# Performance work log

Hardware: AMD Instinct MI355X
Metric: run time of the kernel (lower is better)

Reference implementation:

```python
import jax, jax.numpy as jnp
import numpy as np
import math

N, E, LAT, MUL, HD = 20000, 160000, 128, 16, 32
H = LAT // HD          # 4 heads
D = 9                  # 0e+1o+2e spherical harmonics dim
SLICES = ((0, 1), (1, 4), (4, 9))
TPD = MUL * len(SLICES)


def _mlp(x, W1, b1, W2, b2):
    return jnp.dot(jax.nn.silu(jnp.dot(x, W1) + b1), W2) + b2


def _eq_linear(x, W):
    # block-diagonal per-l channel mixing: x [E, mul, D], W [n_l, mul, mul]
    return jnp.concatenate([jnp.einsum('ji,eim->ejm', W[l], x[:, :, s:t])
                            for l, (s, t) in enumerate(SLICES)], axis=-1)


def _residual(x, x_new, uc):
    co = jax.lax.rsqrt(uc * uc + 1.0)
    return co * x + (uc * co) * x_new


def _vec_rej(feat, dirs):
    d = dirs[:, None, :]
    return feat - (feat * d).sum(-1, keepdims=True) * d


def _so3_ln(x, eps=1e-8):
    # equivariant RMS layernorm per irrep block
    out = []
    for s, t in SLICES:
        blk = x[:, :, s:t]
        rms = jnp.sqrt((blk * blk).sum(-1).mean(-1) + eps)  # [N]
        out.append(blk / rms[:, None, None])
    return jnp.concatenate(out, axis=-1)


def _ln(x, g, b, eps=1e-5):
    mu = x.mean(-1, keepdims=True)
    var = ((x - mu) ** 2).mean(-1, keepdims=True)
    return (x - mu) * jax.lax.rsqrt(var + eps) * g + b


def _forward(h, X, t_ij, spharms, update_coeff, Wtq, Wtk, Wrs_W, Wrs_b, Wq_W, Wq_b, Wk_W, Wk_b, Wre_W, ln_g, ln_b, Wvu,
             gs_W1, gs_b1, gs_W2, gs_b2, gv_W1, gv_b1, gv_W2, gv_b2, gw_W1, gw_b1, gw_W2, gw_b2,
             gt_W1, gt_b1, gt_W2, gt_b2, gsp_W1, gsp_b1, gsp_W2, gsp_b2, md_W1, md_b1, md_W2, md_b2,
             mt_W1, mt_b1, mt_W2, mt_b2, gm_W1, gm_b1, gm_W2, gm_b2,
             edge_center, edge_neighbor, num_nodes):
    uc = update_coeff
    Xn = X[edge_neighbor]                                     # [E, mul, D]
    Xq = _vec_rej(_eq_linear(X[edge_center], Wtq), spharms)
    Xk = _vec_rej(_eq_linear(Xn, Wtk), -spharms)
    # CG scalar contraction (l x l -> 0e, uuu): normalized per-l dot product
    w = jnp.concatenate([(Xq[:, :, s:t] * Xk[:, :, s:t]).sum(-1) / math.sqrt(t - s)
                         for s, t in SLICES], axis=-1)        # [E, 3*mul]
    dt = _mlp(w, gw_W1, gw_b1, gw_W2, gw_b2) * _mlp(t_ij, gt_W1, gt_b1, gt_W2, gt_b2)
    t_ij = _residual(t_ij, dt, uc)
    h_i = h[edge_center]
    h_j = h[edge_neighbor]
    spatial = (t_ij @ Wrs_W + Wrs_b) * _mlp(h_j, gs_W1, gs_b1, gs_W2, gs_b2)
    En = t_ij.shape[0]
    q = (h_i @ Wq_W + Wq_b).reshape(En, H, HD)
    k = (h_j @ Wk_W + Wk_b).reshape(En, H, HD)
    v = _mlp(h_j, gv_W1, gv_b1, gv_W2, gv_b2)
    ta = jax.nn.silu(t_ij @ Wre_W).reshape(En, H, HD)
    alpha = (q * k * ta).sum(-1) / math.sqrt(HD)              # [E, H]
    amax = jax.ops.segment_max(alpha, edge_center, num_segments=num_nodes)
    ex = jnp.exp(alpha - amax[edge_center])
    den = jax.ops.segment_sum(ex, edge_center, num_segments=num_nodes)
    attn = ex / den[edge_center]                              # scatter_softmax
    sea = (attn[:, :, None] * v.reshape(En, H, HD)).reshape(En, LAT)
    combined = sea + spatial
    gates = _mlp(combined, gsp_W1, gsp_b1, gsp_W2, gsp_b2)
    o_s, o_d, o_t = gates[:, :LAT], gates[:, LAT:2 * LAT], gates[:, 2 * LAT:]
    dh = _ln(jax.ops.segment_sum(o_s, edge_center, num_segments=num_nodes), ln_g, ln_b)
    h = _residual(h, dh, uc)
    gd = _mlp(o_d, md_W1, md_b1, md_W2, md_b2)
    gtt = _mlp(o_t, mt_W1, mt_b1, mt_W2, mt_b2)
    dXij = gd[:, :, None] * spharms[:, None, :] + gtt[:, :, None] * Xn
    dX = _so3_ln(jax.ops.segment_sum(dXij, edge_center, num_segments=num_nodes))
    X = _residual(X, dX, uc)
    # EQFF
    Xp = jnp.einsum('nmi,mj->nji', X, Wvu)
    nrm = jnp.sqrt((Xp * Xp).sum(-1) + 1e-12)
    g = _mlp(jnp.concatenate([h, nrm], axis=-1), gm_W1, gm_b1, gm_W2, gm_b2)
    h = h + g[:, :LAT]
    X = X + g[:, LAT:, None] * Xp
    return h, X, t_ij


def setup_inputs() -> dict:
    key = jax.random.key(0)
    ks = jax.random.split(key, 24)

    def mk_mlp(k, din, dout):
        k1, k2 = jax.random.split(k)
        return (jax.random.normal(k1, (din, LAT)) / math.sqrt(din), jnp.zeros((LAT,)),
                jax.random.normal(k2, (LAT, dout)) / math.sqrt(LAT), jnp.zeros((dout,)))

    inp = {
        'h': jax.random.normal(ks[0], (N, LAT)),
        'X': jax.random.normal(ks[1], (N, MUL, D)),
        't_ij': jax.random.normal(ks[2], (E, LAT)),
        'spharms': jax.random.normal(ks[3], (E, D)),
        'update_coeff': jnp.ones((1,), dtype=jnp.float32),
        'Wtq': jax.random.normal(ks[4], (len(SLICES), MUL, MUL)) / math.sqrt(MUL),
        'Wtk': jax.random.normal(ks[5], (len(SLICES), MUL, MUL)) / math.sqrt(MUL),
        'Wrs_W': jax.random.normal(ks[6], (LAT, LAT)) / math.sqrt(LAT),
        'Wrs_b': jnp.zeros((LAT,)),
        'Wq_W': jax.random.normal(ks[7], (LAT, LAT)) / math.sqrt(LAT),
        'Wq_b': jnp.zeros((LAT,)),
        'Wk_W': jax.random.normal(ks[8], (LAT, LAT)) / math.sqrt(LAT),
        'Wk_b': jnp.zeros((LAT,)),
        'Wre_W': jax.random.normal(ks[9], (LAT, LAT)) / math.sqrt(LAT),
        'ln_g': jnp.ones((LAT,)),
        'ln_b': jnp.zeros((LAT,)),
        'Wvu': jax.random.normal(ks[10], (MUL, MUL)) / math.sqrt(MUL),
    }
    for name, din, dout, k in [('gs', LAT, LAT, ks[11]), ('gv', LAT, LAT, ks[12]), ('gw', TPD, LAT, ks[13]),
                               ('gt', LAT, LAT, ks[14]), ('gsp', LAT, 3 * LAT, ks[15]), ('md', LAT, MUL, ks[16]),
                               ('mt', LAT, MUL, ks[17]), ('gm', LAT + MUL, LAT + MUL, ks[18])]:
        W1, b1, W2, b2 = mk_mlp(k, din, dout)
        inp[name + '_W1'], inp[name + '_b1'], inp[name + '_W2'], inp[name + '_b2'] = W1, b1, W2, b2
    inp['edge_center'] = jax.random.randint(ks[19], (E,), 0, N)
    inp['edge_neighbor'] = jax.random.randint(ks[20], (E,), 0, N)
    inp['num_nodes'] = N
    return inp


def reference(h, X, t_ij, spharms, update_coeff, Wtq, Wtk, Wrs_W, Wrs_b, Wq_W, Wq_b, Wk_W, Wk_b, Wre_W, ln_g, ln_b, Wvu,
              gs_W1, gs_b1, gs_W2, gs_b2, gv_W1, gv_b1, gv_W2, gv_b2, gw_W1, gw_b1, gw_W2, gw_b2,
              gt_W1, gt_b1, gt_W2, gt_b2, gsp_W1, gsp_b1, gsp_W2, gsp_b2, md_W1, md_b1, md_W2, md_b2,
              mt_W1, mt_b1, mt_W2, mt_b2, gm_W1, gm_b1, gm_W2, gm_b2,
              edge_center, edge_neighbor, num_nodes):
    return _forward(h, X, t_ij, spharms, update_coeff, Wtq, Wtk, Wrs_W, Wrs_b, Wq_W, Wq_b, Wk_W, Wk_b, Wre_W, ln_g, ln_b, Wvu,
                    gs_W1, gs_b1, gs_W2, gs_b2, gv_W1, gv_b1, gv_W2, gv_b2, gw_W1, gw_b1, gw_W2, gw_b2,
                    gt_W1, gt_b1, gt_W2, gt_b2, gsp_W1, gsp_b1, gsp_W2, gsp_b2, md_W1, md_b1, md_W2, md_b2,
                    mt_W1, mt_b1, mt_W2, mt_b2, gm_W1, gm_b1, gm_W2, gm_b2,
                    edge_center, edge_neighbor, num_nodes)
```

## Files before the change

kernel.cpp:

```cpp
#include <hip/hip_runtime.h>
#include <math.h>

#define N_NODES 20000
#define E_EDGES 160000
#define LAT 128
#define MUL 16
#define DD 9
#define TPD 48

#define WS_Q      ((size_t)0)
#define WS_K      (WS_Q + (size_t)N_NODES*LAT)
#define WS_V      (WS_K + (size_t)N_NODES*LAT)
#define WS_S      (WS_V + (size_t)N_NODES*LAT)
#define WS_W48    (WS_S + (size_t)N_NODES*LAT)
#define WS_SPATB  (WS_W48 + (size_t)E_EDGES*TPD)
#define WS_ALPHA  (WS_SPATB + (size_t)E_EDGES*LAT/2)
#define WS_ZERO   (WS_ALPHA + (size_t)E_EDGES*4)
#define WS_AMAX   WS_ZERO
#define WS_DEN    (WS_AMAX + (size_t)N_NODES*4)
#define WS_HSUM   (WS_DEN + (size_t)N_NODES*4)
#define WS_NDX    (WS_HSUM + (size_t)N_NODES*LAT)
#define WS_END    (WS_NDX + (size_t)N_NODES*MUL*DD)
#define ZERO_CNT  (WS_END - WS_ZERO)
#define WS_WB     WS_END

#define WOFF_WQ   0
#define WOFF_WK   16384
#define WOFF_GV1  32768
#define WOFF_GV2  49152
#define WOFF_GS1  65536
#define WOFF_GS2  81920
#define WOFF_GW1  98304
#define WOFF_GW2  106496
#define WOFF_GT1  122880
#define WOFF_GT2  139264
#define WOFF_WRS  155648
#define WOFF_WRE  172032
#define WOFF_GSP1 188416
#define WOFF_GSP2 204800
#define WOFF_MD1  253952
#define WOFF_MD2  270336
#define WOFF_MT1  272384
#define WOFF_MT2  288768
#define WB_TOTAL  290816

#define DEVI __device__ __forceinline__

typedef short short8 __attribute__((ext_vector_type(8)));
typedef float f32x4 __attribute__((ext_vector_type(4)));

DEVI float frcp(float x){ return __builtin_amdgcn_rcpf(x); }
DEVI float silu_f(float x){ return x * frcp(1.f + __expf(-x)); }
DEVI unsigned int fmap(float x){ unsigned int b=__float_as_uint(x); return (b&0x80000000u)? ~b : (b|0x80000000u); }
DEVI float funmap(unsigned int u){ return (u&0x80000000u)? __uint_as_float(u&0x7fffffffu) : __uint_as_float(~u); }
DEVI unsigned short f2b(float f){ unsigned int u=__float_as_uint(f); return (unsigned short)((u + 0x7fffu + ((u>>16)&1u))>>16); }
DEVI float b2f(unsigned short u){ return __uint_as_float(((unsigned int)u)<<16); }

DEVI f32x4 mfma16(short8 a, short8 b, f32x4 c){
  return __builtin_amdgcn_mfma_f32_16x16x32_bf16(a,b,c,0,0,0);
}

template<int KB>
DEVI void mm_tile2(const unsigned short* act, int strideUS, const unsigned short* Wp,
                   int ntile, int m, int quad, f32x4* acc){
  const unsigned short* wp = Wp + (size_t)ntile*KB*512 + (size_t)quad*128 + m*8;
  const unsigned short* a0 = act + m*strideUS + quad*8;
  const unsigned short* a1 = a0 + 16*strideUS;
  #pragma unroll
  for (int kb=0;kb<KB;++kb){
    short8 bfr = *(const short8*)(wp + (size_t)kb*512);
    short8 af0 = *(const short8*)(a0 + kb*32);
    short8 af1 = *(const short8*)(a1 + kb*32);
    acc[0]=mfma16(af0,bfr,acc[0]);
    acc[1]=mfma16(af1,bfr,acc[1]);
  }
}

template<int KB>
DEVI void mm_tile1(const unsigned short* act, int strideUS, const unsigned short* Wp,
                   int mtbase, int m, int quad, f32x4& acc){
  const unsigned short* wp = Wp + (size_t)quad*128 + m*8;
  const unsigned short* a0 = act + (mtbase*16+m)*strideUS + quad*8;
  #pragma unroll
  for (int kb=0;kb<KB;++kb){
    short8 bfr = *(const short8*)(wp + (size_t)kb*512);
    short8 af  = *(const short8*)(a0 + kb*32);
    acc=mfma16(af,bfr,acc);
  }
}

template<int R, int KD, int LDSTRIDE>
DEVI void mm_acc(const float* src, const float* __restrict__ W, int wstride, int t, float* acc){
  #pragma unroll 2
  for (int k=0;k<KD;k+=4){
    float4 xv[R];
    #pragma unroll
    for (int r=0;r<R;++r) xv[r] = *(const float4*)(src + r*LDSTRIDE + k);
    #pragma unroll
    for (int kk=0;kk<4;++kk){
      float wk = W[(size_t)(k+kk)*wstride + t];
      #pragma unroll
      for (int r=0;r<R;++r) acc[r] += ((const float*)&xv[r])[kk]*wk;
    }
  }
}

__global__ void k0_zero(float* __restrict__ z){
  size_t i = (size_t)blockIdx.x*256 + threadIdx.x;
  if (i < ZERO_CNT) z[i] = 0.f;
}

__global__ __launch_bounds__(256) void k_pack(
  const float* __restrict__ Wq,const float* __restrict__ Wk,
  const float* __restrict__ gv1,const float* __restrict__ gv2,
  const float* __restrict__ gs1,const float* __restrict__ gs2,
  const float* __restrict__ gw1,const float* __restrict__ gw2,
  const float* __restrict__ gt1,const float* __restrict__ gt2,
  const float* __restrict__ Wrs,const float* __restrict__ Wre,
  const float* __restrict__ gsp1,const float* __restrict__ gsp2,
  const float* __restrict__ md1,const float* __restrict__ md2,
  const float* __restrict__ mt1,const float* __restrict__ mt2,
  unsigned short* __restrict__ dst)
{
  int i = blockIdx.x*256 + threadIdx.x;
  if (i >= WB_TOTAL) return;
  const int off[19] = {0,16384,32768,49152,65536,81920,98304,106496,122880,139264,
                       155648,172032,188416,204800,253952,270336,272384,288768,290816};
  int mi=0;
  while (i >= off[mi+1]) ++mi;
  int li = i - off[mi];
  int N = (mi==13)?384:((mi==15||mi==17)?16:128);
  int Ksrc = (mi==6)?48:128;
  int KB = (mi==6)?2:4;
  int j = li&7; int t = li>>3;
  int n_in = t&15; t>>=4;
  int quad = t&3; t>>=2;
  int k_block = t % KB; int n_tile = t / KB;
  int k = k_block*32 + quad*8 + j;
  int n = n_tile*16 + n_in;
  const float* src;
  switch(mi){
    case 0: src=Wq; break;  case 1: src=Wk; break;
    case 2: src=gv1; break; case 3: src=gv2; break;
    case 4: src=gs1; break; case 5: src=gs2; break;
    case 6: src=gw1; break; case 7: src=gw2; break;
    case 8: src=gt1; break; case 9: src=gt2; break;
    case 10: src=Wrs; break; case 11: src=Wre; break;
    case 12: src=gsp1; break; case 13: src=gsp2; break;
    case 14: src=md1; break; case 15: src=md2; break;
    default: src=(mi==16)?mt1:mt2; break;
  }
  float v = (k < Ksrc) ? src[(size_t)k*N + n] : 0.f;
  dst[i] = f2b(v);
}

__global__ __launch_bounds__(256) void k1_node(const float* __restrict__ h,
  const unsigned short* __restrict__ WB,
  const float* __restrict__ Wq_b,const float* __restrict__ Wk_b,
  const float* __restrict__ gv_b1,const float* __restrict__ gv_b2,
  const float* __restrict__ gs_b1,const float* __restrict__ gs_b2,
  float* __restrict__ ws)
{
  __shared__ __align__(16) unsigned short B0[32*136], B1[32*136];
  const int tid=threadIdx.x, lane=tid&63, w=tid>>6, m=lane&15, quad=lane>>4;
  const int n0=blockIdx.x*32;
  for (int idx=tid; idx<4096; idx+=256){ int r=idx>>7,c=idx&127;
    B0[r*136+c]=f2b(h[(size_t)(n0+r)*128+c]); }
  __syncthreads();
  f32x4 z4 = {0.f,0.f,0.f,0.f};
  { f32x4 acc[2][2]={{z4,z4},{z4,z4}};
    #pragma unroll
    for(int i=0;i<2;++i) mm_tile2<4>(B0,136,WB+WOFF_WQ, w*2+i, m, quad, acc[i]);
    #pragma unroll
    for(int i=0;i<2;++i){ int col=(w*2+i)*16+m; float bv=Wq_b[col];
      #pragma unroll
      for(int mt=0;mt<2;++mt)
        #pragma unroll
        for(int r=0;r<4;++r){ int row=mt*16+quad*4+r;
          ws[WS_Q+(size_t)(n0+row)*128+col]=acc[i][mt][r]+bv; } } }
  { f32x4 acc[2][2]={{z4,z4},{z4,z4}};
    #pragma unroll
    for(int i=0;i<2;++i) mm_tile2<4>(B0,136,WB+WOFF_WK, w*2+i, m, quad, acc[i]);
    #pragma unroll
    for(int i=0;i<2;++i){ int col=(w*2+i)*16+m; float bv=Wk_b[col];
      #pragma unroll
      for(int mt=0;mt<2;++mt)
        #pragma unroll
        for(int r=0;r<4;++r){ int row=mt*16+quad*4+r;
          ws[WS_K+(size_t)(n0+row)*128+col]=acc[i][mt][r]+bv; } } }
  { f32x4 acc[2][2]={{z4,z4},{z4,z4}};
    #pragma unroll
    for(int i=0;i<2;++i) mm_tile2<4>(B0,136,WB+WOFF_GV1, w*2+i, m, quad, acc[i]);
    #pragma unroll
    for(int i=0;i<2;++i){ int col=(w*2+i)*16+m; float bv=gv_b1[col];
      #pragma unroll
      for(int mt=0;mt<2;++mt)
        #pragma unroll
        for(int r=0;r<4;++r) B1[(mt*16+quad*4+r)*136+col]=f2b(silu_f(acc[i][mt][r]+bv)); } }
  __syncthreads();
  { f32x4 acc[2][2]={{z4,z4},{z4,z4}};
    #pragma unroll
    for(int i=0;i<2;++i) mm_tile2<4>(B1,136,WB+WOFF_GV2, w*2+i, m, quad, acc[i]);
    #pragma unroll
    for(int i=0;i<2;++i){ int col=(w*2+i)*16+m; float bv=gv_b2[col];
      #pragma unroll
      for(int mt=0;mt<2;++mt)
        #pragma unroll
        for(int r=0;r<4;++r){ int row=mt*16+quad*4+r;
          ws[WS_V+(size_t)(n0+row)*128+col]=acc[i][mt][r]+bv; } } }
  __syncthreads();
  { f32x4 acc[2][2]={{z4,z4},{z4,z4}};
    #pragma unroll
    for(int i=0;i<2;++i) mm_tile2<4>(B0,136,WB+WOFF_GS1, w*2+i, m, quad, acc[i]);
    #pragma unroll
    for(int i=0;i<2;++i){ int col=(w*2+i)*16+m; float bv=gs_b1[col];
      #pragma unroll
      for(int mt=0;mt<2;++mt)
        #pragma unroll
        for(int r=0;r<4;++r) B1[(mt*16+quad*4+r)*136+col]=f2b(silu_f(acc[i][mt][r]+bv)); } }
  __syncthreads();
  { f32x4 acc[2][2]={{z4,z4},{z4,z4}};
    #pragma unroll
    for(int i=0;i<2;++i) mm_tile2<4>(B1,136,WB+WOFF_GS2, w*2+i, m, quad, acc[i]);
    #pragma unroll
    for(int i=0;i<2;++i){ int col=(w*2+i)*16+m; float bv=gs_b2[col];
      #pragma unroll
      for(int mt=0;mt<2;++mt)
        #pragma unroll
        for(int r=0;r<4;++r){ int row=mt*16+quad*4+r;
          ws[WS_S+(size_t)(n0+row)*128+col]=acc[i][mt][r]+bv; } } }
}

__global__ __launch_bounds__(256) void k2_edge_w(
  const float* __restrict__ Xin, const float* __restrict__ sph,
  const float* __restrict__ Wtq, const float* __restrict__ Wtk,
  const int* __restrict__ ec, const int* __restrict__ en, float* __restrict__ ws)
{
  __shared__ float xc[16][144], xn[16][144], sphL[16][9];
  __shared__ float wq[768], wkk[768];
  __shared__ int ceI[16], nbI[16];
  const int tid=threadIdx.x, e0=blockIdx.x*16;
  if (tid<16){ ceI[tid]=ec[e0+tid]; nbI[tid]=en[e0+tid]; }
  for (int idx=tid; idx<768; idx+=256){ wq[idx]=Wtq[idx]; wkk[idx]=Wtk[idx]; }
  __syncthreads();
  for (int idx=tid; idx<2304; idx+=256){ int r=idx/144,c=idx%144;
    xc[r][c]=Xin[(size_t)ceI[r]*144+c]; xn[r][c]=Xin[(size_t)nbI[r]*144+c]; }
  if (tid<144){ int r=tid/9,c=tid%9; sphL[r][c]=sph[(size_t)(e0+r)*9+c]; }
  __syncthreads();
  const int el=tid>>4, j=tid&15;
  float xq[9], xk[9];
  const int ss[3]={0,1,4}, se[3]={1,4,9};
  #pragma unroll
  for (int l=0;l<3;++l){
    for (int mm2=ss[l]; mm2<se[l]; ++mm2){
      float aq=0.f, ak=0.f;
      #pragma unroll
      for (int i=0;i<16;++i){
        float wql = wq[l*256 + j*16 + i], wkl = wkk[l*256 + j*16 + i];
        aq += wql*xc[el][i*9+mm2];
        ak += wkl*xn[el][i*9+mm2];
      }
      xq[mm2]=aq; xk[mm2]=ak;
    }
  }
  float dq=0.f, dk=0.f;
  #pragma unroll
  for (int d=0; d<9; ++d){ dq += xq[d]*sphL[el][d]; dk += xk[d]*sphL[el][d]; }
  #pragma unroll
  for (int d=0; d<9; ++d){ xq[d] -= dq*sphL[el][d]; xk[d] -= dk*sphL[el][d]; }
  const float isc[3] = {1.f, 0.5773502691896258f, 0.4472135954999579f};
  #pragma unroll
  for (int l=0;l<3;++l){
    float s=0.f;
    for (int mm2=ss[l]; mm2<se[l]; ++mm2) s += xq[mm2]*xk[mm2];
    ws[WS_W48 + (size_t)(e0+el)*TPD + l*16 + j] = s*isc[l];
  }
}

__global__ __launch_bounds__(256) void k3_edge_t(
  const float* __restrict__ t_in, const int* __restrict__ ec, const int* __restrict__ en,
  const unsigned short* __restrict__ WB,
  const float* __restrict__ gw_b1,const float* __restrict__ gw_b2,
  const float* __restrict__ gt_b1,const float* __restrict__ gt_b2,
  const float* __restrict__ Wrs_b,
  const float* __restrict__ ucp, float* __restrict__ ws, float* __restrict__ outT)
{
  __shared__ __align__(16) unsigned short tin_b[32*136], hid_b[32*136], tnw_b[32*136], wb_b[32*72];
  __shared__ int ceI[32], nbI[32];
  const int tid=threadIdx.x, lane=tid&63, w=tid>>6, m=lane&15, quad=lane>>4;
  const int e0=blockIdx.x*32;
  if (tid<32){ ceI[tid]=ec[e0+tid]; nbI[tid]=en[e0+tid]; }
  for (int idx=tid; idx<4096; idx+=256){
    int r=idx>>7, c=idx&127;
    tin_b[r*136+c] = f2b(t_in[(size_t)(e0+r)*128+c]);
  }
  for (int idx=tid; idx<2048; idx+=256){
    int r=idx>>6, c=idx&63;
    wb_b[r*72+c] = (c<48)? f2b(ws[WS_W48+(size_t)(e0+r)*TPD+c]) : (unsigned short)0;
  }
  __syncthreads();
  const float uc=ucp[0], co=rsqrtf(uc*uc+1.f), ucco=uc*co;
  f32x4 z4 = {0.f,0.f,0.f,0.f};
  { f32x4 acc[2][2]={{z4,z4},{z4,z4}};
    #pragma unroll
    for(int i=0;i<2;++i) mm_tile2<2>(wb_b,72,WB+WOFF_GW1, w*2+i, m, quad, acc[i]);
    #pragma unroll
    for(int i=0;i<2;++i){ int col=(w*2+i)*16+m; float bv=gw_b1[col];
      #pragma unroll
      for(int mt=0;mt<2;++mt)
        #pragma unroll
        for(int r=0;r<4;++r) hid_b[(mt*16+quad*4+r)*136+col]=f2b(silu_f(acc[i][mt][r]+bv)); } }
  __syncthreads();
  f32x4 accw[2][2]={{z4,z4},{z4,z4}};
  #pragma unroll
  for(int i=0;i<2;++i) mm_tile2<4>(hid_b,136,WB+WOFF_GW2, w*2+i, m, quad, accw[i]);
  __syncthreads();
  { f32x4 acc[2][2]={{z4,z4},{z4,z4}};
    #pragma unroll
    for(int i=0;i<2;++i) mm_tile2<4>(tin_b,136,WB+WOFF_GT1, w*2+i, m, quad, acc[i]);
    #pragma unroll
    for(int i=0;i<2;++i){ int col=(w*2+i)*16+m; float bv=gt_b1[col];
      #pragma unroll
      for(int mt=0;mt<2;++mt)
        #pragma unroll
        for(int r=0;r<4;++r) hid_b[(mt*16+quad*4+r)*136+col]=f2b(silu_f(acc[i][mt][r]+bv)); } }
  __syncthreads();
  { f32x4 acct[2][2]={{z4,z4},{z4,z4}};
    #pragma unroll
    for(int i=0;i<2;++i) mm_tile2<4>(hid_b,136,WB+WOFF_GT2, w*2+i, m, quad, acct[i]);
    #pragma unroll
    for(int i=0;i<2;++i){ int col=(w*2+i)*16+m; float bw=gw_b2[col], bt=gt_b2[col];
      #pragma unroll
      for(int mt=0;mt<2;++mt)
        #pragma unroll
        for(int r=0;r<4;++r){ int row=mt*16+quad*4+r;
          float dt=(accw[i][mt][r]+bw)*(acct[i][mt][r]+bt);
          float tn=co*b2f(tin_b[row*136+col]) + ucco*dt;
          tnw_b[row*136+col]=f2b(tn);
          outT[(size_t)(e0+row)*128+col]=tn; } } }
  __syncthreads();
  unsigned short* spatB = (unsigned short*)(ws+WS_SPATB);
  { f32x4 acc[2][2]={{z4,z4},{z4,z4}};
    #pragma unroll
    for(int i=0;i<2;++i) mm_tile2<4>(tnw_b,136,WB+WOFF_WRS, w*2+i, m, quad, acc[i]);
    #pragma unroll
    for(int i=0;i<2;++i){ int col=(w*2+i)*16+m; float bv=Wrs_b[col];
      #pragma unroll
      for(int mt=0;mt<2;++mt)
        #pragma unroll
        for(int r=0;r<4;++r){ int row=mt*16+quad*4+r;
          float sv=ws[WS_S+(size_t)nbI[row]*128+col];
          spatB[(size_t)(e0+row)*128+col]=f2b((acc[i][mt][r]+bv)*sv); } } }
  { f32x4 acc[2][2]={{z4,z4},{z4,z4}};
    #pragma unroll
    for(int i=0;i<2;++i) mm_tile2<4>(tnw_b,136,WB+WOFF_WRE, w*2+i, m, quad, acc[i]);
    unsigned int* amaxu=(unsigned int*)(ws+WS_AMAX);
    const float* Qp=ws+WS_Q; const float* Kp=ws+WS_K;
    #pragma unroll
    for(int mt=0;mt<2;++mt)
      #pragma unroll
      for(int r=0;r<4;++r){ int row=mt*16+quad*4+r;
        int ce=ceI[row], nb=nbI[row];
        float p=0.f;
        #pragma unroll
        for(int i=0;i<2;++i){ int col=(w*2+i)*16+m;
          float qk = Qp[(size_t)ce*128+col]*Kp[(size_t)nb*128+col];
          p += qk*silu_f(acc[i][mt][r]); }
        p += __shfl_xor(p,1); p += __shfl_xor(p,2); p += __shfl_xor(p,4); p += __shfl_xor(p,8);
        if (m==0){
          float aval = p * 0.17677669529663687f;
          int e=e0+row;
          ws[WS_ALPHA+(size_t)e*4+w]=aval;
          atomicMax(&amaxu[(size_t)ce*4+w], fmap(aval));
        } } }
}

__global__ __launch_bounds__(256) void k4_softmax(const int* __restrict__ ec, float* __restrict__ ws){
  int i = blockIdx.x*256 + threadIdx.x;
  if (i >= E_EDGES*4) return;
  int e = i>>2, hh = i&3;
  int c = ec[e];
  float a = ws[WS_ALPHA + i];
  const unsigned int* amaxu = (const unsigned int*)(ws + WS_AMAX);
  float am = funmap(amaxu[(size_t)c*4+hh]);
  float exv = __expf(a - am);
  ws[WS_ALPHA + i] = exv;
  atomicAdd(&ws[WS_DEN + (size_t)c*4 + hh], exv);
}

__global__ __launch_bounds__(256) void k5_edge_gate(
  const float* __restrict__ Xin, const float* __restrict__ sph,
  const int* __restrict__ ec, const int* __restrict__ en,
  const unsigned short* __restrict__ WB,
  const float* __restrict__ gsp_b1,const float* __restrict__ gsp_b2,
  const float* __restrict__ md_b1,const float* __restrict__ md_b2,
  const float* __restrict__ mt_b1,const float* __restrict__ mt_b2,
  float* __restrict__ ws)
{
  __shared__ __align__(16) unsigned short B0[32*136], B1[32*136], B2[32*136];
  __shared__ float gdL[32*16], gtL[32*16], attnL[32*4];
  __shared__ int ceI[32], nbI[32];
  const int tid=threadIdx.x, lane=tid&63, w=tid>>6, m=lane&15, quad=lane>>4;
  const int e0=blockIdx.x*32;
  if (tid<32){ ceI[tid]=ec[e0+tid]; nbI[tid]=en[e0+tid]; }
  __syncthreads();
  if (tid<128){ int r=tid>>2, hh=tid&3;
    attnL[tid] = ws[WS_ALPHA+(size_t)(e0+r)*4+hh] * frcp(ws[WS_DEN+(size_t)ceI[r]*4+hh]); }
  __syncthreads();
  const float* Vp=ws+WS_V;
  const unsigned short* spatB=(const unsigned short*)(ws+WS_SPATB);
  for (int idx=tid; idx<4096; idx+=256){ int r=idx>>7,c=idx&127;
    float v = attnL[r*4+(c>>5)]*Vp[(size_t)nbI[r]*128+c] + b2f(spatB[(size_t)(e0+r)*128+c]);
    B0[r*136+c]=f2b(v); }
  __syncthreads();
  f32x4 z4 = {0.f,0.f,0.f,0.f};
  { f32x4 acc[2][2]={{z4,z4},{z4,z4}};
    #pragma unroll
    for(int i=0;i<2;++i) mm_tile2<4>(B0,136,WB+WOFF_GSP1, w*2+i, m, quad, acc[i]);
    #pragma unroll
    for(int i=0;i<2;++i){ int col=(w*2+i)*16+m; float bv=gsp_b1[col];
      #pragma unroll
      for(int mt=0;mt<2;++mt)
        #pragma unroll
        for(int r=0;r<4;++r) B1[(mt*16+quad*4+r)*136+col]=f2b(silu_f(acc[i][mt][r]+bv)); } }
  __syncthreads();
  { f32x4 acc[3][2][2];
    #pragma unroll
    for(int g2=0;g2<3;++g2)
      #pragma unroll
      for(int i=0;i<2;++i){ acc[g2][i][0]=z4; acc[g2][i][1]=z4; }
    #pragma unroll
    for(int g2=0;g2<3;++g2)
      #pragma unroll
      for(int i=0;i<2;++i)
        mm_tile2<4>(B1,136,WB+WOFF_GSP2, g2*8+w*2+i, m, quad, acc[g2][i]);
    float* hsum=ws+WS_HSUM;
    #pragma unroll
    for(int i=0;i<2;++i){ int col=(w*2+i)*16+m;
      float bS=gsp_b2[col], bD=gsp_b2[128+col], bT=gsp_b2[256+col];
      #pragma unroll
      for(int mt=0;mt<2;++mt)
        #pragma unroll
        for(int r=0;r<4;++r){ int row=mt*16+quad*4+r;
          atomicAdd(&hsum[(size_t)ceI[row]*128+col], acc[0][i][mt][r]+bS);
          B0[row*136+col]=f2b(acc[1][i][mt][r]+bD);
          B2[row*136+col]=f2b(acc[2][i][mt][r]+bT); } } }
  __syncthreads();
  { f32x4 acc[2][2]={{z4,z4},{z4,z4}};
    #pragma unroll
    for(int i=0;i<2;++i) mm_tile2<4>(B0,136,WB+WOFF_MD1, w*2+i, m, quad, acc[i]);
    #pragma unroll
    for(int i=0;i<2;++i){ int col=(w*2+i)*16+m; float bv=md_b1[col];
      #pragma unroll
      for(int mt=0;mt<2;++mt)
        #pragma unroll
        for(int r=0;r<4;++r) B1[(mt*16+quad*4+r)*136+col]=f2b(silu_f(acc[i][mt][r]+bv)); } }
  __syncthreads();
  { f32x4 acc[2][2]={{z4,z4},{z4,z4}};
    #pragma unroll
    for(int i=0;i<2;++i) mm_tile2<4>(B2,136,WB+WOFF_MT1, w*2+i, m, quad, acc[i]);
    #pragma unroll
    for(int i=0;i<2;++i){ int col=(w*2+i)*16+m; float bv=mt_b1[col];
      #pragma unroll
      for(int mt=0;mt<2;++mt)
        #pragma unroll
        for(int r=0;r<4;++r) B0[(mt*16+quad*4+r)*136+col]=f2b(silu_f(acc[i][mt][r]+bv)); } }
  __syncthreads();
  { if (w<2){
      f32x4 a=z4; mm_tile1<4>(B1,136,WB+WOFF_MD2, w, m, quad, a);
      #pragma unroll
      for(int r=0;r<4;++r) gdL[(w*16+quad*4+r)*16+m]=a[r]+md_b2[m];
    } else {
      f32x4 a=z4; mm_tile1<4>(B0,136,WB+WOFF_MT2, w-2, m, quad, a);
      #pragma unroll
      for(int r=0;r<4;++r) gtL[((w-2)*16+quad*4+r)*16+m]=a[r]+mt_b2[m];
    } }
  __syncthreads();
  float* ndx=ws+WS_NDX;
  for (int idx=tid; idx<4608; idx+=256){
    int r=idx/144, c=idx-r*144; int mm2=c/9, d=c-mm2*9;
    float val = gdL[r*16+mm2]*sph[(size_t)(e0+r)*9+d] + gtL[r*16+mm2]*Xin[(size_t)nbI[r]*144+c];
    atomicAdd(&ndx[(size_t)ceI[r]*144+c], val);
  }
}

__global__ __launch_bounds__(128) void k6_node(
  const float* __restrict__ h, const float* __restrict__ Xin,
  const float* __restrict__ ln_g,const float* __restrict__ ln_b,
  const float* __restrict__ Wvu,
  const float* __restrict__ gm_W1,const float* __restrict__ gm_b1,
  const float* __restrict__ gm_W2,const float* __restrict__ gm_b2,
  const float* __restrict__ ucp, const float* __restrict__ ws,
  float* __restrict__ outH, float* __restrict__ outX)
{
  __shared__ float cat[4][144], dxb[4][144], xnw[4][144], xp[4][144], hid[4][LAT];
  __shared__ float red[4][2][2], rinv[4][3], gX[4][16], wvu[256];
  const int t=threadIdx.x, n0=blockIdx.x*4;
  const float* hsum=ws+WS_HSUM; const float* ndx=ws+WS_NDX;
  const float uc=ucp[0], co=rsqrtf(uc*uc+1.f), ucco=uc*co;
  for (int idx=t; idx<256; idx+=128) wvu[idx]=Wvu[idx];
  for (int idx=t; idx<576; idx+=128){ int r=idx/144,c=idx%144; dxb[r][c]=ndx[(size_t)(n0+r)*144+c]; }
  float xv_[4];
  #pragma unroll
  for (int r=0;r<4;++r){
    float x=hsum[(size_t)(n0+r)*LAT+t]; xv_[r]=x;
    float s=x, ss=x*x;
    for (int off=32; off; off>>=1){ s+=__shfl_down(s,off,64); ss+=__shfl_down(ss,off,64); }
    if ((t&63)==0){ red[r][t>>6][0]=s; red[r][t>>6][1]=ss; }
  }
  __syncthreads();
  #pragma unroll
  for (int r=0;r<4;++r){
    float s=red[r][0][0]+red[r][1][0], ss=red[r][0][1]+red[r][1][1];
    float mu=s*(1.f/128.f), var=ss*(1.f/128.f)-mu*mu;
    float dh=(xv_[r]-mu)*rsqrtf(var+1e-5f)*ln_g[t]+ln_b[t];
    cat[r][t]=co*h[(size_t)(n0+r)*LAT+t]+ucco*dh;
  }
  if (t<12){
    int r=t/3, l=t-r*3;
    int s0 = (l==0)?0:((l==1)?1:4);
    int s1 = (l==0)?1:((l==1)?4:9);
    float sum=0.f;
    for (int mm2=0;mm2<16;++mm2)
      for (int d=s0;d<s1;++d){ float v=dxb[r][mm2*9+d]; sum+=v*v; }
    rinv[r][l]=rsqrtf(sum*(1.f/16.f)+1e-8f);
  }
  __syncthreads();
  for (int idx=t; idx<144; idx+=128){
    int d=idx%9; int l=(d==0)?0:((d<4)?1:2);
    #pragma unroll
    for (int r=0;r<4;++r)
      xnw[r][idx]=co*Xin[(size_t)(n0+r)*144+idx]+ucco*dxb[r][idx]*rinv[r][l];
  }
  __syncthreads();
  for (int idx=t; idx<144; idx+=128){
    int j=idx/9, i=idx-j*9;
    #pragma unroll
    for (int r=0;r<4;++r){
      float a=0.f;
      #pragma unroll
      for (int mm2=0;mm2<16;++mm2) a+=xnw[r][mm2*9+i]*wvu[mm2*16+j];
      xp[r][idx]=a;
    }
  }
  __syncthreads();
  if (t<64){ int r=t>>4, j=t&15; float s=1e-12f;
    #pragma unroll
    for (int i=0;i<9;++i){ float v=xp[r][j*9+i]; s+=v*v; }
    cat[r][128+j]=sqrtf(s); }
  __syncthreads();
  { float acc[4]; float b=gm_b1[t];
    #pragma unroll
    for(int r=0;r<4;++r)acc[r]=b;
    mm_acc<4,144,144>(&cat[0][0],gm_W1,LAT,t,acc);
    #pragma unroll
    for(int r=0;r<4;++r) hid[r][t]=silu_f(acc[r]); }
  __syncthreads();
  { float acc[4]; float b=gm_b2[t];
    #pragma unroll
    for(int r=0;r<4;++r)acc[r]=b;
    mm_acc<4,LAT,LAT>(&hid[0][0],gm_W2,144,t,acc);
    #pragma unroll
    for(int r=0;r<4;++r) outH[(size_t)(n0+r)*LAT+t]=cat[r][t]+acc[r]; }
  if (t<16){ float acc[4]; float b=gm_b2[128+t];
    #pragma unroll
    for(int r=0;r<4;++r)acc[r]=b;
    for (int k=0;k<LAT;++k){ float wk=gm_W2[(size_t)k*144+128+t];
      #pragma unroll
      for(int r=0;r<4;++r) acc[r]+=hid[r][k]*wk; }
    #pragma unroll
    for(int r=0;r<4;++r) gX[r][t]=acc[r]; }
  __syncthreads();
  for (int idx=t; idx<144; idx+=128){
    int j=idx/9;
    #pragma unroll
    for (int r=0;r<4;++r)
      outX[(size_t)(n0+r)*144+idx]=xnw[r][idx]+gX[r][j]*xp[r][idx];
  }
}

extern "C" void kernel_launch(void* const* d_in, const int* in_sizes, int n_in,
                              void* d_out, int out_size, void* d_ws, size_t ws_size,
                              hipStream_t stream)
{
  const float* h      = (const float*)d_in[0];
  const float* X      = (const float*)d_in[1];
  const float* t_ij   = (const float*)d_in[2];
  const float* sph    = (const float*)d_in[3];
  const float* ucp    = (const float*)d_in[4];
  const float* Wtq    = (const float*)d_in[5];
  const float* Wtk    = (const float*)d_in[6];
  const float* Wrs_W  = (const float*)d_in[7];
  const float* Wrs_b  = (const float*)d_in[8];
  const float* Wq_W   = (const float*)d_in[9];
  const float* Wq_b   = (const float*)d_in[10];
  const float* Wk_W   = (const float*)d_in[11];
  const float* Wk_b   = (const float*)d_in[12];
  const float* Wre_W  = (const float*)d_in[13];
  const float* ln_g   = (const float*)d_in[14];
  const float* ln_b   = (const float*)d_in[15];
  const float* Wvu    = (const float*)d_in[16];
  const float* gs_W1=(const float*)d_in[17], *gs_b1=(const float*)d_in[18],
             *gs_W2=(const float*)d_in[19], *gs_b2=(const float*)d_in[20];
  const float* gv_W1=(const float*)d_in[21], *gv_b1=(const float*)d_in[22],
             *gv_W2=(const float*)d_in[23], *gv_b2=(const float*)d_in[24];
  const float* gw_W1=(const float*)d_in[25], *gw_b1=(const float*)d_in[26],
             *gw_W2=(const float*)d_in[27], *gw_b2=(const float*)d_in[28];
  const float* gt_W1=(const float*)d_in[29], *gt_b1=(const float*)d_in[30],
             *gt_W2=(const float*)d_in[31], *gt_b2=(const float*)d_in[32];
  const float* gsp_W1=(const float*)d_in[33], *gsp_b1=(const float*)d_in[34],
             *gsp_W2=(const float*)d_in[35], *gsp_b2=(const float*)d_in[36];
  const float* md_W1=(const float*)d_in[37], *md_b1=(const float*)d_in[38],
             *md_W2=(const float*)d_in[39], *md_b2=(const float*)d_in[40];
  const float* mt_W1=(const float*)d_in[41], *mt_b1=(const float*)d_in[42],
             *mt_W2=(const float*)d_in[43], *mt_b2=(const float*)d_in[44];
  const float* gm_W1=(const float*)d_in[45], *gm_b1=(const float*)d_in[46],
             *gm_W2=(const float*)d_in[47], *gm_b2=(const float*)d_in[48];
  const int* ec = (const int*)d_in[49];
  const int* en = (const int*)d_in[50];
  (void)in_sizes; (void)n_in; (void)out_size; (void)ws_size;

  float* ws   = (float*)d_ws;
  unsigned short* WB = (unsigned short*)(ws + WS_WB);
  float* outH = (float*)d_out;
  float* outX = outH + (size_t)N_NODES*LAT;
  float* outT = outX + (size_t)N_NODES*MUL*DD;

  k0_zero<<<dim3((unsigned)((ZERO_CNT+255)/256)), dim3(256), 0, stream>>>(ws + WS_ZERO);
  k_pack<<<dim3((WB_TOTAL+255)/256), dim3(256), 0, stream>>>(
      Wq_W,Wk_W, gv_W1,gv_W2, gs_W1,gs_W2, gw_W1,gw_W2, gt_W1,gt_W2,
      Wrs_W,Wre_W, gsp_W1,gsp_W2, md_W1,md_W2, mt_W1,mt_W2, WB);
  k1_node<<<dim3(N_NODES/32), dim3(256), 0, stream>>>(h, WB, Wq_b, Wk_b,
      gv_b1,gv_b2, gs_b1,gs_b2, ws);
  k2_edge_w<<<dim3(E_EDGES/16), dim3(256), 0, stream>>>(X, sph, Wtq, Wtk, ec, en, ws);
  k3_edge_t<<<dim3(E_EDGES/32), dim3(256), 0, stream>>>(t_ij, ec, en, WB,
      gw_b1,gw_b2, gt_b1,gt_b2, Wrs_b, ucp, ws, outT);
  k4_softmax<<<dim3((E_EDGES*4)/256), dim3(256), 0, stream>>>(ec, ws);
  k5_edge_gate<<<dim3(E_EDGES/32), dim3(256), 0, stream>>>(X, sph, ec, en, WB,
      gsp_b1,gsp_b2, md_b1,md_b2, mt_b1,mt_b2, ws);
  k6_node<<<dim3(N_NODES/4), dim3(128), 0, stream>>>(h, X, ln_g, ln_b, Wvu,
      gm_W1,gm_b1,gm_W2,gm_b2, ucp, ws, outH, outX);
}
```

Measured before the change: 813.7 us.

## Store node Q/K/V/S in bf16 and widen edge kernels to 512 threads

Node projections Q, K, V and S are now written as bf16 instead of fp32, which halves the bytes moved by the per-edge gathers in the edge kernels. The two edge kernels k3 and k5 now run with 512 threads (8 waves), each wave owning one 16-column tile instead of two, to raise parallelism per block. The per-head attention logit reduction in k3 now goes through shared-memory atomics before a single atomicMax per edge and head. Rounding Q, K, V and S to bf16 lowers precision, and the larger blocks may reduce occupancy.

```diff
diff --git a/kernel.cpp b/kernel.cpp
--- a/kernel.cpp
+++ b/kernel.cpp
@@ -8,11 +8,11 @@
 #define DD 9
 #define TPD 48
 
-#define WS_Q      ((size_t)0)
-#define WS_K      (WS_Q + (size_t)N_NODES*LAT)
-#define WS_V      (WS_K + (size_t)N_NODES*LAT)
-#define WS_S      (WS_V + (size_t)N_NODES*LAT)
-#define WS_W48    (WS_S + (size_t)N_NODES*LAT)
+#define WS_QB     ((size_t)0)
+#define WS_KBN    (WS_QB  + (size_t)N_NODES*64)
+#define WS_VBN    (WS_KBN + (size_t)N_NODES*64)
+#define WS_SBN    (WS_VBN + (size_t)N_NODES*64)
+#define WS_W48    (WS_SBN + (size_t)N_NODES*64)
 #define WS_SPATB  (WS_W48 + (size_t)E_EDGES*TPD)
 #define WS_ALPHA  (WS_SPATB + (size_t)E_EDGES*LAT/2)
 #define WS_ZERO   (WS_ALPHA + (size_t)E_EDGES*4)
@@ -159,7 +159,8 @@
   const float* __restrict__ Wq_b,const float* __restrict__ Wk_b,
   const float* __restrict__ gv_b1,const float* __restrict__ gv_b2,
   const float* __restrict__ gs_b1,const float* __restrict__ gs_b2,
-  float* __restrict__ ws)
+  unsigned short* __restrict__ Qb, unsigned short* __restrict__ Kb,
+  unsigned short* __restrict__ Vb, unsigned short* __restrict__ Sb)
 {
   __shared__ __align__(16) unsigned short B0[32*136], B1[32*136];
   const int tid=threadIdx.x, lane=tid&63, w=tid>>6, m=lane&15, quad=lane>>4;
@@ -177,7 +178,7 @@
       for(int mt=0;mt<2;++mt)
         #pragma unroll
         for(int r=0;r<4;++r){ int row=mt*16+quad*4+r;
-          ws[WS_Q+(size_t)(n0+row)*128+col]=acc[i][mt][r]+bv; } } }
+          Qb[(size_t)(n0+row)*128+col]=f2b(acc[i][mt][r]+bv); } } }
   { f32x4 acc[2][2]={{z4,z4},{z4,z4}};
     #pragma unroll
     for(int i=0;i<2;++i) mm_tile2<4>(B0,136,WB+WOFF_WK, w*2+i, m, quad, acc[i]);
@@ -187,7 +188,7 @@
       for(int mt=0;mt<2;++mt)
         #pragma unroll
         for(int r=0;r<4;++r){ int row=mt*16+quad*4+r;
-          ws[WS_K+(size_t)(n0+row)*128+col]=acc[i][mt][r]+bv; } } }
+          Kb[(size_t)(n0+row)*128+col]=f2b(acc[i][mt][r]+bv); } } }
   { f32x4 acc[2][2]={{z4,z4},{z4,z4}};
     #pragma unroll
     for(int i=0;i<2;++i) mm_tile2<4>(B0,136,WB+WOFF_GV1, w*2+i, m, quad, acc[i]);
@@ -207,7 +208,7 @@
       for(int mt=0;mt<2;++mt)
         #pragma unroll
         for(int r=0;r<4;++r){ int row=mt*16+quad*4+r;
-          ws[WS_V+(size_t)(n0+row)*128+col]=acc[i][mt][r]+bv; } } }
+          Vb[(size_t)(n0+row)*128+col]=f2b(acc[i][mt][r]+bv); } } }
   __syncthreads();
   { f32x4 acc[2][2]={{z4,z4},{z4,z4}};
     #pragma unroll
@@ -228,7 +229,7 @@
       for(int mt=0;mt<2;++mt)
         #pragma unroll
         for(int r=0;r<4;++r){ int row=mt*16+quad*4+r;
-          ws[WS_S+(size_t)(n0+row)*128+col]=acc[i][mt][r]+bv; } } }
+          Sb[(size_t)(n0+row)*128+col]=f2b(acc[i][mt][r]+bv); } } }
 }
 
 __global__ __launch_bounds__(256) void k2_edge_w(
@@ -277,102 +278,96 @@
   }
 }
 
-__global__ __launch_bounds__(256) void k3_edge_t(
+__global__ __launch_bounds__(512,8) void k3_edge_t(
   const float* __restrict__ t_in, const int* __restrict__ ec, const int* __restrict__ en,
   const unsigned short* __restrict__ WB,
   const float* __restrict__ gw_b1,const float* __restrict__ gw_b2,
   const float* __restrict__ gt_b1,const float* __restrict__ gt_b2,
   const float* __restrict__ Wrs_b,
+  const unsigned short* __restrict__ Qb, const unsigned short* __restrict__ Kb,
+  const unsigned short* __restrict__ Sb,
   const float* __restrict__ ucp, float* __restrict__ ws, float* __restrict__ outT)
 {
   __shared__ __align__(16) unsigned short tin_b[32*136], hid_b[32*136], tnw_b[32*136], wb_b[32*72];
+  __shared__ float alphaP[128];
   __shared__ int ceI[32], nbI[32];
   const int tid=threadIdx.x, lane=tid&63, w=tid>>6, m=lane&15, quad=lane>>4;
   const int e0=blockIdx.x*32;
   if (tid<32){ ceI[tid]=ec[e0+tid]; nbI[tid]=en[e0+tid]; }
-  for (int idx=tid; idx<4096; idx+=256){
+  if (tid>=384) alphaP[tid-384]=0.f;
+  for (int idx=tid; idx<4096; idx+=512){
     int r=idx>>7, c=idx&127;
     tin_b[r*136+c] = f2b(t_in[(size_t)(e0+r)*128+c]);
   }
-  for (int idx=tid; idx<2048; idx+=256){
+  for (int idx=tid; idx<2048; idx+=512){
     int r=idx>>6, c=idx&63;
     wb_b[r*72+c] = (c<48)? f2b(ws[WS_W48+(size_t)(e0+r)*TPD+c]) : (unsigned short)0;
   }
   __syncthreads();
   const float uc=ucp[0], co=rsqrtf(uc*uc+1.f), ucco=uc*co;
+  const int col = w*16+m;
   f32x4 z4 = {0.f,0.f,0.f,0.f};
-  { f32x4 acc[2][2]={{z4,z4},{z4,z4}};
-    #pragma unroll
-    for(int i=0;i<2;++i) mm_tile2<2>(wb_b,72,WB+WOFF_GW1, w*2+i, m, quad, acc[i]);
-    #pragma unroll
-    for(int i=0;i<2;++i){ int col=(w*2+i)*16+m; float bv=gw_b1[col];
-      #pragma unroll
-      for(int mt=0;mt<2;++mt)
-        #pragma unroll
-        for(int r=0;r<4;++r) hid_b[(mt*16+quad*4+r)*136+col]=f2b(silu_f(acc[i][mt][r]+bv)); } }
-  __syncthreads();
-  f32x4 accw[2][2]={{z4,z4},{z4,z4}};
-  #pragma unroll
-  for(int i=0;i<2;++i) mm_tile2<4>(hid_b,136,WB+WOFF_GW2, w*2+i, m, quad, accw[i]);
-  __syncthreads();
-  { f32x4 acc[2][2]={{z4,z4},{z4,z4}};
-    #pragma unroll
-    for(int i=0;i<2;++i) mm_tile2<4>(tin_b,136,WB+WOFF_GT1, w*2+i, m, quad, acc[i]);
-    #pragma unroll
-    for(int i=0;i<2;++i){ int col=(w*2+i)*16+m; float bv=gt_b1[col];
-      #pragma unroll
-      for(int mt=0;mt<2;++mt)
-        #pragma unroll
-        for(int r=0;r<4;++r) hid_b[(mt*16+quad*4+r)*136+col]=f2b(silu_f(acc[i][mt][r]+bv)); } }
-  __syncthreads();
-  { f32x4 acct[2][2]={{z4,z4},{z4,z4}};
-    #pragma unroll
-    for(int i=0;i<2;++i) mm_tile2<4>(hid_b,136,WB+WOFF_GT2, w*2+i, m, quad, acct[i]);
-    #pragma unroll
-    for(int i=0;i<2;++i){ int col=(w*2+i)*16+m; float bw=gw_b2[col], bt=gt_b2[col];
-      #pragma unroll
-      for(int mt=0;mt<2;++mt)
-        #pragma unroll
-        for(int r=0;r<4;++r){ int row=mt*16+quad*4+r;
-          float dt=(accw[i][mt][r]+bw)*(acct[i][mt][r]+bt);
-          float tn=co*b2f(tin_b[row*136+col]) + ucco*dt;
-          tnw_b[row*136+col]=f2b(tn);
-          outT[(size_t)(e0+row)*128+col]=tn; } } }
+  { f32x4 acc[2]={z4,z4};
+    mm_tile2<2>(wb_b,72,WB+WOFF_GW1, w, m, quad, acc);
+    float bv=gw_b1[col];
+    #pragma unroll
+    for(int mt=0;mt<2;++mt)
+      #pragma unroll
+      for(int r=0;r<4;++r) hid_b[(mt*16+quad*4+r)*136+col]=f2b(silu_f(acc[mt][r]+bv)); }
+  __syncthreads();
+  f32x4 accw[2]={z4,z4};
+  mm_tile2<4>(hid_b,136,WB+WOFF_GW2, w, m, quad, accw);
+  __syncthreads();
+  { f32x4 acc[2]={z4,z4};
+    mm_tile2<4>(tin_b,136,WB+WOFF_GT1, w, m, quad, acc);
+    float bv=gt_b1[col];
+    #pragma unroll
+    for(int mt=0;mt<2;++mt)
+      #pragma unroll
+      for(int r=0;r<4;++r) hid_b[(mt*16+quad*4+r)*136+col]=f2b(silu_f(acc[mt][r]+bv)); }
+  __syncthreads();
+  { f32x4 acct[2]={z4,z4};
+    mm_tile2<4>(hid_b,136,WB+WOFF_GT2, w, m, quad, acct);
+    float bw=gw_b2[col], bt=gt_b2[col];
+    #pragma unroll
+    for(int mt=0;mt<2;++mt)
+      #pragma unroll
+      for(int r=0;r<4;++r){ int row=mt*16+quad*4+r;
+        float dt=(accw[mt][r]+bw)*(acct[mt][r]+bt);
+        float tn=co*b2f(tin_b[row*136+col]) + ucco*dt;
+        tnw_b[row*136+col]=f2b(tn);
+        outT[(size_t)(e0+row)*128+col]=tn; } }
   __syncthreads();
   unsigned short* spatB = (unsigned short*)(ws+WS_SPATB);
-  { f32x4 acc[2][2]={{z4,z4},{z4,z4}};
-    #pragma unroll
-    for(int i=0;i<2;++i) mm_tile2<4>(tnw_b,136,WB+WOFF_WRS, w*2+i, m, quad, acc[i]);
-    #pragma unroll
-    for(int i=0;i<2;++i){ int col=(w*2+i)*16+m; float bv=Wrs_b[col];
-      #pragma unroll
-      for(int mt=0;mt<2;++mt)
-        #pragma unroll
-        for(int r=0;r<4;++r){ int row=mt*16+quad*4+r;
-          float sv=ws[WS_S+(size_t)nbI[row]*128+col];
-          spatB[(size_t)(e0+row)*128+col]=f2b((acc[i][mt][r]+bv)*sv); } } }
-  { f32x4 acc[2][2]={{z4,z4},{z4,z4}};
-    #pragma unroll
-    for(int i=0;i<2;++i) mm_tile2<4>(tnw_b,136,WB+WOFF_WRE, w*2+i, m, quad, acc[i]);
+  { f32x4 acc[2]={z4,z4};
+    mm_tile2<4>(tnw_b,136,WB+WOFF_WRS, w, m, quad, acc);
+    float bv=Wrs_b[col];
+    #pragma unroll
+    for(int mt=0;mt<2;++mt)
+      #pragma unroll
+      for(int r=0;r<4;++r){ int row=mt*16+quad*4+r;
+        float sv=b2f(Sb[(size_t)nbI[row]*128+col]);
+        spatB[(size_t)(e0+row)*128+col]=f2b((acc[mt][r]+bv)*sv); } }
+  { f32x4 acc[2]={z4,z4};
+    mm_tile2<4>(tnw_b,136,WB+WOFF_WRE, w, m, quad, acc);
+    #pragma unroll
+    for(int mt=0;mt<2;++mt)
+      #pragma unroll
+      for(int r=0;r<4;++r){ int row=mt*16+quad*4+r;
+        float qv=b2f(Qb[(size_t)ceI[row]*128+col]);
+        float kv=b2f(Kb[(size_t)nbI[row]*128+col]);
+        float p = qv*kv*silu_f(acc[mt][r]);
+        p += __shfl_xor(p,1); p += __shfl_xor(p,2); p += __shfl_xor(p,4); p += __shfl_xor(p,8);
+        if (m==0) atomicAdd(&alphaP[row*4+(w>>1)], p);
+      } }
+  __syncthreads();
+  if (tid<128){
+    int row=tid>>2, hh=tid&3;
+    float aval = alphaP[tid] * 0.17677669529663687f;
+    ws[WS_ALPHA+(size_t)(e0+row)*4+hh]=aval;
     unsigned int* amaxu=(unsigned int*)(ws+WS_AMAX);
-    const float* Qp=ws+WS_Q; const float* Kp=ws+WS_K;
-    #pragma unroll
-    for(int mt=0;mt<2;++mt)
-      #pragma unroll
-      for(int r=0;r<4;++r){ int row=mt*16+quad*4+r;
-        int ce=ceI[row], nb=nbI[row];
-        float p=0.f;
-        #pragma unroll
-        for(int i=0;i<2;++i){ int col=(w*2+i)*16+m;
-          float qk = Qp[(size_t)ce*128+col]*Kp[(size_t)nb*128+col];
-          p += qk*silu_f(acc[i][mt][r]); }
-        p += __shfl_xor(p,1); p += __shfl_xor(p,2); p += __shfl_xor(p,4); p += __shfl_xor(p,8);
-        if (m==0){
-          float aval = p * 0.17677669529663687f;
-          int e=e0+row;
-          ws[WS_ALPHA+(size_t)e*4+w]=aval;
-          atomicMax(&amaxu[(size_t)ce*4+w], fmap(aval));
-        } } }
+    atomicMax(&amaxu[(size_t)ceI[row]*4+hh], fmap(aval));
+  }
 }
 
 __global__ __launch_bounds__(256) void k4_softmax(const int* __restrict__ ec, float* __restrict__ ws){
@@ -388,13 +383,14 @@
   atomicAdd(&ws[WS_DEN + (size_t)c*4 + hh], exv);
 }
 
-__global__ __launch_bounds__(256) void k5_edge_gate(
+__global__ __launch_bounds__(512,8) void k5_edge_gate(
   const float* __restrict__ Xin, const float* __restrict__ sph,
   const int* __restrict__ ec, const int* __restrict__ en,
   const unsigned short* __restrict__ WB,
   const float* __restrict__ gsp_b1,const float* __restrict__ gsp_b2,
   const float* __restrict__ md_b1,const float* __restrict__ md_b2,
   const float* __restrict__ mt_b1,const float* __restrict__ mt_b2,
+  const unsigned short* __restrict__ Vb,
   float* __restrict__ ws)
 {
   __shared__ __align__(16) unsigned short B0[32*136], B1[32*136], B2[32*136];
@@ -407,77 +403,65 @@
   if (tid<128){ int r=tid>>2, hh=tid&3;
     attnL[tid] = ws[WS_ALPHA+(size_t)(e0+r)*4+hh] * frcp(ws[WS_DEN+(size_t)ceI[r]*4+hh]); }
   __syncthreads();
-  const float* Vp=ws+WS_V;
   const unsigned short* spatB=(const unsigned short*)(ws+WS_SPATB);
-  for (int idx=tid; idx<4096; idx+=256){ int r=idx>>7,c=idx&127;
-    float v = attnL[r*4+(c>>5)]*Vp[(size_t)nbI[r]*128+c] + b2f(spatB[(size_t)(e0+r)*128+c]);
+  for (int idx=tid; idx<4096; idx+=512){ int r=idx>>7,c=idx&127;
+    float v = attnL[r*4+(c>>5)]*b2f(Vb[(size_t)nbI[r]*128+c]) + b2f(spatB[(size_t)(e0+r)*128+c]);
     B0[r*136+c]=f2b(v); }
   __syncthreads();
+  const int col = w*16+m;
   f32x4 z4 = {0.f,0.f,0.f,0.f};
-  { f32x4 acc[2][2]={{z4,z4},{z4,z4}};
-    #pragma unroll
-    for(int i=0;i<2;++i) mm_tile2<4>(B0,136,WB+WOFF_GSP1, w*2+i, m, quad, acc[i]);
-    #pragma unroll
-    for(int i=0;i<2;++i){ int col=(w*2+i)*16+m; float bv=gsp_b1[col];
-      #pragma unroll
-      for(int mt=0;mt<2;++mt)
-        #pragma unroll
-        for(int r=0;r<4;++r) B1[(mt*16+quad*4+r)*136+col]=f2b(silu_f(acc[i][mt][r]+bv)); } }
-  __syncthreads();
-  { f32x4 acc[3][2][2];
+  { f32x4 acc[2]={z4,z4};
+    mm_tile2<4>(B0,136,WB+WOFF_GSP1, w, m, quad, acc);
+    float bv=gsp_b1[col];
+    #pragma unroll
+    for(int mt=0;mt<2;++mt)
+      #pragma unroll
+      for(int r=0;r<4;++r) B1[(mt*16+quad*4+r)*136+col]=f2b(silu_f(acc[mt][r]+bv)); }
+  __syncthreads();
+  { f32x4 acc[3][2];
+    #pragma unroll
+    for(int g2=0;g2<3;++g2){ acc[g2][0]=z4; acc[g2][1]=z4; }
     #pragma unroll
     for(int g2=0;g2<3;++g2)
-      #pragma unroll
-      for(int i=0;i<2;++i){ acc[g2][i][0]=z4; acc[g2][i][1]=z4; }
-    #pragma unroll
-    for(int g2=0;g2<3;++g2)
-      #pragma unroll
-      for(int i=0;i<2;++i)
-        mm_tile2<4>(B1,136,WB+WOFF_GSP2, g2*8+w*2+i, m, quad, acc[g2][i]);
+      mm_tile2<4>(B1,136,WB+WOFF_GSP2, g2*8+w, m, quad, acc[g2]);
     float* hsum=ws+WS_HSUM;
-    #pragma unroll
-    for(int i=0;i<2;++i){ int col=(w*2+i)*16+m;
-      float bS=gsp_b2[col], bD=gsp_b2[128+col], bT=gsp_b2[256+col];
-      #pragma unroll
-      for(int mt=0;mt<2;++mt)
-        #pragma unroll
-        for(int r=0;r<4;++r){ int row=mt*16+quad*4+r;
-          atomicAdd(&hsum[(size_t)ceI[row]*128+col], acc[0][i][mt][r]+bS);
-          B0[row*136+col]=f2b(acc[1][i][mt][r]+bD);
-          B2[row*136+col]=f2b(acc[2][i][mt][r]+bT); } } }
-  __syncthreads();
-  { f32x4 acc[2][2]={{z4,z4},{z4,z4}};
-    #pragma unroll
-    for(int i=0;i<2;++i) mm_tile2<4>(B0,136,WB+WOFF_MD1, w*2+i, m, quad, acc[i]);
-    #pragma unroll
-    for(int i=0;i<2;++i){ int col=(w*2+i)*16+m; float bv=md_b1[col];
-      #pragma unroll
-      for(int mt=0;mt<2;++mt)
-        #pragma unroll
-        for(int r=0;r<4;++r) B1[(mt*16+quad*4+r)*136+col]=f2b(silu_f(acc[i][mt][r]+bv)); } }
-  __syncthreads();
-  { f32x4 acc[2][2]={{z4,z4},{z4,z4}};
-    #pragma unroll
-    for(int i=0;i<2;++i) mm_tile2<4>(B2,136,WB+WOFF_MT1, w*2+i, m, quad, acc[i]);
-    #pragma unroll
-    for(int i=0;i<2;++i){ int col=(w*2+i)*16+m; float bv=mt_b1[col];
-      #pragma unroll
-      for(int mt=0;mt<2;++mt)
-        #pragma unroll
-        for(int r=0;r<4;++r) B0[(mt*16+quad*4+r)*136+col]=f2b(silu_f(acc[i][mt][r]+bv)); } }
+    float bS=gsp_b2[col], bD=gsp_b2[128+col], bT=gsp_b2[256+col];
+    #pragma unroll
+    for(int mt=0;mt<2;++mt)
+      #pragma unroll
+      for(int r=0;r<4;++r){ int row=mt*16+quad*4+r;
+        atomicAdd(&hsum[(size_t)ceI[row]*128+col], acc[0][mt][r]+bS);
+        B0[row*136+col]=f2b(acc[1][mt][r]+bD);
+        B2[row*136+col]=f2b(acc[2][mt][r]+bT); } }
+  __syncthreads();
+  { f32x4 acc[2]={z4,z4};
+    mm_tile2<4>(B0,136,WB+WOFF_MD1, w, m, quad, acc);
+    float bv=md_b1[col];
+    #pragma unroll
+    for(int mt=0;mt<2;++mt)
+      #pragma unroll
+      for(int r=0;r<4;++r) B1[(mt*16+quad*4+r)*136+col]=f2b(silu_f(acc[mt][r]+bv)); }
+  __syncthreads();
+  { f32x4 acc[2]={z4,z4};
+    mm_tile2<4>(B2,136,WB+WOFF_MT1, w, m, quad, acc);
+    float bv=mt_b1[col];
+    #pragma unroll
+    for(int mt=0;mt<2;++mt)
+      #pragma unroll
+      for(int r=0;r<4;++r) B0[(mt*16+quad*4+r)*136+col]=f2b(silu_f(acc[mt][r]+bv)); }
   __syncthreads();
   { if (w<2){
       f32x4 a=z4; mm_tile1<4>(B1,136,WB+WOFF_MD2, w, m, quad, a);
       #pragma unroll
       for(int r=0;r<4;++r) gdL[(w*16+quad*4+r)*16+m]=a[r]+md_b2[m];
-    } else {
+    } else if (w<4){
       f32x4 a=z4; mm_tile1<4>(B0,136,WB+WOFF_MT2, w-2, m, quad, a);
       #pragma unroll
       for(int r=0;r<4;++r) gtL[((w-2)*16+quad*4+r)*16+m]=a[r]+mt_b2[m];
     } }
   __syncthreads();
   float* ndx=ws+WS_NDX;
-  for (int idx=tid; idx<4608; idx+=256){
+  for (int idx=tid; idx<4608; idx+=512){
     int r=idx/144, c=idx-r*144; int mm2=c/9, d=c-mm2*9;
     float val = gdL[r*16+mm2]*sph[(size_t)(e0+r)*9+d] + gtL[r*16+mm2]*Xin[(size_t)nbI[r]*144+c];
     atomicAdd(&ndx[(size_t)ceI[r]*144+c], val);
@@ -622,6 +606,10 @@
 
   float* ws   = (float*)d_ws;
   unsigned short* WB = (unsigned short*)(ws + WS_WB);
+  unsigned short* Qb = (unsigned short*)(ws + WS_QB);
+  unsigned short* Kb = (unsigned short*)(ws + WS_KBN);
+  unsigned short* Vb = (unsigned short*)(ws + WS_VBN);
+  unsigned short* Sb = (unsigned short*)(ws + WS_SBN);
   float* outH = (float*)d_out;
   float* outX = outH + (size_t)N_NODES*LAT;
   float* outT = outX + (size_t)N_NODES*MUL*DD;
@@ -631,13 +619,13 @@
       Wq_W,Wk_W, gv_W1,gv_W2, gs_W1,gs_W2, gw_W1,gw_W2, gt_W1,gt_W2,
       Wrs_W,Wre_W, gsp_W1,gsp_W2, md_W1,md_W2, mt_W1,mt_W2, WB);
   k1_node<<<dim3(N_NODES/32), dim3(256), 0, stream>>>(h, WB, Wq_b, Wk_b,
-      gv_b1,gv_b2, gs_b1,gs_b2, ws);
+      gv_b1,gv_b2, gs_b1,gs_b2, Qb, Kb, Vb, Sb);
   k2_edge_w<<<dim3(E_EDGES/16), dim3(256), 0, stream>>>(X, sph, Wtq, Wtk, ec, en, ws);
-  k3_edge_t<<<dim3(E_EDGES/32), dim3(256), 0, stream>>>(t_ij, ec, en, WB,
-      gw_b1,gw_b2, gt_b1,gt_b2, Wrs_b, ucp, ws, outT);
+  k3_edge_t<<<dim3(E_EDGES/32), dim3(512), 0, stream>>>(t_ij, ec, en, WB,
+      gw_b1,gw_b2, gt_b1,gt_b2, Wrs_b, Qb, Kb, Sb, ucp, ws, outT);
   k4_softmax<<<dim3((E_EDGES*4)/256), dim3(256), 0, stream>>>(ec, ws);
-  k5_edge_gate<<<dim3(E_EDGES/32), dim3(256), 0, stream>>>(X, sph, ec, en, WB,
-      gsp_b1,gsp_b2, md_b1,md_b2, mt_b1,mt_b2, ws);
+  k5_edge_gate<<<dim3(E_EDGES/32), dim3(512), 0, stream>>>(X, sph, ec, en, WB,
+      gsp_b1,gsp_b2, md_b1,md_b2, mt_b1,mt_b2, Vb, ws);
   k6_node<<<dim3(N_NODES/4), dim3(128), 0, stream>>>(h, X, ln_g, ln_b, Wvu,
       gm_W1,gm_b1,gm_W2,gm_b2, ucp, ws, outH, outX);
 }
```

Result: no change. 818.0 us (+0.5%).
